# Kernel optimization log

Measured on AMD Instinct MI355X. Metric: run time of the kernel, lower is better.

## Reference

```python
import jax, jax.numpy as jnp
import numpy as np

D_MODEL = 1024
N_HEADS = 16
D_HEAD = D_MODEL // N_HEADS
D_FF = 4096
B, T = 2, 2048


def layer_norm(x, gamma, beta, eps=1e-5):
    mu = jnp.mean(x, axis=-1, keepdims=True)
    var = jnp.var(x, axis=-1, keepdims=True)
    return (x - mu) * jax.lax.rsqrt(var + eps) * gamma + beta


def setup_inputs() -> dict:
    key = jax.random.key(0)
    ks = jax.random.split(key, 8)
    s = D_MODEL ** -0.5
    return {
        "x": jax.random.normal(ks[0], (B, T, D_MODEL), dtype=jnp.float32),
        "w_qkv": jax.random.normal(ks[1], (D_MODEL, 3 * D_MODEL), dtype=jnp.float32) * s,
        "w_out": jax.random.normal(ks[2], (D_MODEL, D_MODEL), dtype=jnp.float32) * s,
        "ln1_g": jnp.ones((D_MODEL,), jnp.float32),
        "ln1_b": jnp.zeros((D_MODEL,), jnp.float32),
        "ln2_g": jnp.ones((D_MODEL,), jnp.float32),
        "ln2_b": jnp.zeros((D_MODEL,), jnp.float32),
        "w1": jax.random.normal(ks[3], (D_MODEL, D_FF), dtype=jnp.float32) * s,
        "b1": jnp.zeros((D_FF,), jnp.float32),
        "w2": jax.random.normal(ks[4], (D_FF, D_MODEL), dtype=jnp.float32) * (D_FF ** -0.5),
        "b2": jnp.zeros((D_MODEL,), jnp.float32),
    }


def reference(x, w_qkv, w_out, ln1_g, ln1_b, ln2_g, ln2_b, w1, b1, w2, b2):
    Bb, Tt, C = x.shape
    h = layer_norm(x, ln1_g, ln1_b)
    qkv = h @ w_qkv  # [B,T,3C]
    q, k, v = jnp.split(qkv, 3, axis=-1)

    def heads(t):  # [B,T,C] -> [B,H,T,Dh]
        return t.reshape(Bb, Tt, N_HEADS, D_HEAD).transpose(0, 2, 1, 3)

    q, k, v = heads(q), heads(k), heads(v)
    scale = D_HEAD ** -0.5
    attn = jnp.einsum("bhqd,bhkd->bhqk", q, k) * scale
    causal = jnp.tril(jnp.ones((Tt, Tt), dtype=bool))
    attn = jnp.where(causal[None, None], attn, -jnp.inf)
    attn = jax.nn.softmax(attn, axis=-1)
    out = jnp.einsum("bhqk,bhkd->bhqd", attn, v)
    out = out.transpose(0, 2, 1, 3).reshape(Bb, Tt, C)
    x = x + out @ w_out
    h2 = layer_norm(x, ln2_g, ln2_b)
    ff = jax.nn.gelu(h2 @ w1 + b1, approximate=False) @ w2 + b2
    return x + ff
```

## Files before the change

kernel.cpp:

```cpp
#include <hip/hip_runtime.h>
#include <hip/hip_bf16.h>
#include <cstdint>

#define DM 1024
#define DFF 4096
#define NB 2
#define TT 2048
#define NH 16
#define DH 64

typedef unsigned short u16;
typedef __bf16 bf16x8 __attribute__((ext_vector_type(8)));
typedef float f32x4 __attribute__((ext_vector_type(4)));

__device__ __forceinline__ u16 f2b(float f) {
    union { float f; unsigned u; } v; v.f = f;
    unsigned u = v.u;
    return (u16)((u + 0x7FFFu + ((u >> 16) & 1u)) >> 16);
}

__device__ __forceinline__ float b2f(u16 u) {
    union { unsigned x; float f; } v;
    v.x = ((unsigned)u) << 16;
    return v.f;
}

__device__ __forceinline__ unsigned cvtpk(float a, float b) {
    unsigned r;
    asm("v_cvt_pk_bf16_f32 %0, %1, %2" : "=v"(r) : "v"(a), "v"(b));
    return r;
}

__device__ __forceinline__ float gelu_fast(float z) {
    const float u = z * z;
    const float w = z * __builtin_fmaf(u, 0.10294324f, 2.3022082f);
    const float e = exp2f(w);
    const float r = __builtin_amdgcn_rcpf(1.0f + e);
    return z - z * r;
}

__device__ __forceinline__ f32x4 mfma_bf16(bf16x8 a, bf16x8 b, f32x4 c) {
    return __builtin_amdgcn_mfma_f32_16x16x32_bf16(a, b, c, 0, 0, 0);
}

__device__ __forceinline__ void gload_lds16(const void* g, void* l) {
    __builtin_amdgcn_global_load_lds((const __attribute__((address_space(1))) unsigned int*)g,
                                     (__attribute__((address_space(3))) unsigned int*)l, 16, 0, 0);
}

__global__ __launch_bounds__(256) void transW(const float* __restrict__ W, u16* __restrict__ Wt,
                                              int K, int N) {
    __shared__ float t[32][33];
    int tx = threadIdx.x & 31, ty = threadIdx.x >> 5;
    int k0 = blockIdx.y * 32, n0 = blockIdx.x * 32;
#pragma unroll
    for (int j = 0; j < 4; ++j)
        t[ty + 8 * j][tx] = W[(size_t)(k0 + ty + 8 * j) * N + n0 + tx];
    __syncthreads();
#pragma unroll
    for (int j = 0; j < 4; ++j)
        Wt[(size_t)(n0 + ty + 8 * j) * K + k0 + tx] = f2b(t[tx][ty + 8 * j]);
}

__global__ __launch_bounds__(256) void ln_kernel(const float* __restrict__ X,
                                                 const float* __restrict__ g,
                                                 const float* __restrict__ bt,
                                                 u16* __restrict__ H) {
    int row = blockIdx.x, tid = threadIdx.x;
    float4 v = ((const float4*)(X + (size_t)row * DM))[tid];
    float s = v.x + v.y + v.z + v.w;
    float ss = v.x * v.x + v.y * v.y + v.z * v.z + v.w * v.w;
#pragma unroll
    for (int off = 32; off >= 1; off >>= 1) {
        s += __shfl_xor(s, off);
        ss += __shfl_xor(ss, off);
    }
    __shared__ float sb[8];
    int w = tid >> 6, lane = tid & 63;
    if (lane == 0) { sb[w] = s; sb[4 + w] = ss; }
    __syncthreads();
    s = sb[0] + sb[1] + sb[2] + sb[3];
    ss = sb[4] + sb[5] + sb[6] + sb[7];
    float mu = s * (1.0f / DM);
    float var = ss * (1.0f / DM) - mu * mu;
    float rstd = rsqrtf(var + 1e-5f);
    float4 gv = ((const float4*)g)[tid];
    float4 bv = ((const float4*)bt)[tid];
    uint2 hv;
    hv.x = cvtpk((v.x - mu) * rstd * gv.x + bv.x, (v.y - mu) * rstd * gv.y + bv.y);
    hv.y = cvtpk((v.z - mu) * rstd * gv.z + bv.z, (v.w - mu) * rstd * gv.w + bv.w);
    ((uint2*)(H + (size_t)row * DM))[tid] = hv;
}

__global__ __launch_bounds__(256) void add3_kernel(float* __restrict__ out,
                                                   const u16* __restrict__ p1,
                                                   const u16* __restrict__ p2,
                                                   const u16* __restrict__ p3, int n4) {
    int idx = blockIdx.x * 256 + threadIdx.x;
    const int stride = gridDim.x * 256;
    for (; idx < n4; idx += stride) {
        float4 a = ((const float4*)out)[idx];
        ushort4 b1 = ((const ushort4*)p1)[idx];
        ushort4 b2 = ((const ushort4*)p2)[idx];
        ushort4 b3 = ((const ushort4*)p3)[idx];
        a.x += b2f(b1.x) + b2f(b2.x) + b2f(b3.x);
        a.y += b2f(b1.y) + b2f(b2.y) + b2f(b3.y);
        a.z += b2f(b1.z) + b2f(b2.z) + b2f(b3.z);
        a.w += b2f(b1.w) + b2f(b2.w) + b2f(b3.w);
        ((float4*)out)[idx] = a;
    }
}

template <int MODE>
__global__ __launch_bounds__(512, 2) void gemm256(
    const u16* __restrict__ A, const u16* __restrict__ Bt, int M, int N, int K,
    u16* __restrict__ oq, u16* __restrict__ ok, u16* __restrict__ vt,
    const float* __restrict__ bias, u16* __restrict__ outbf) {
    __shared__ __align__(16) u16 Alds[2][256][64];
    __shared__ __align__(16) u16 Blds[2][256][64];
    const int tid = threadIdx.x;
    const int lane = tid & 63, w = tid >> 6;
    const int wm = w >> 2, wn = w & 3;
    const int l15 = lane & 15, lg = lane >> 4;
    int bid = blockIdx.x + gridDim.x * blockIdx.y;
    const int nwg = gridDim.x * gridDim.y;
    bid = (bid & 7) * (nwg >> 3) + (bid >> 3);
    const int bm = (bid / gridDim.x) * 256, bn = (bid % gridDim.x) * 256;
    const int srow = tid >> 3, pch = tid & 7;
    const int lc = pch ^ (srow & 7);

    const u16* Ap = A + (size_t)(bm + srow) * K + lc * 8;
    const u16* Bp = Bt + (size_t)(bn + srow) * K + lc * 8;

    f32x4 acc[8][4] = {};
    bf16x8 bf[4][2];
    const int NT = K >> 6;

#define SA256(buf, t)                                                           \
    {                                                                           \
        _Pragma("unroll") for (int j = 0; j < 4; ++j)                           \
            gload_lds16(Ap + (size_t)(64 * j) * K + (t) * 64,                   \
                        &Alds[buf][srow + 64 * j][pch * 8]);                    \
    }
#define SB256(buf, t)                                                           \
    {                                                                           \
        _Pragma("unroll") for (int j = 0; j < 4; ++j)                           \
            gload_lds16(Bp + (size_t)(64 * j) * K + (t) * 64,                   \
                        &Blds[buf][srow + 64 * j][pch * 8]);                    \
    }

#define PHASE(BUF, P, STAGE, WAIT)                                              \
    {                                                                           \
        bf16x8 af[2][2];                                                        \
        _Pragma("unroll") for (int i = 0; i < 2; ++i) {                         \
            const int row = wm * 128 + (2 * (P) + i) * 16 + l15;                \
            _Pragma("unroll") for (int ks = 0; ks < 2; ++ks)                    \
                af[i][ks] =                                                     \
                    *(const bf16x8*)&Alds[BUF][row][((ks * 4 + lg) ^ (row & 7)) * 8]; \
        }                                                                       \
        if constexpr ((P) == 0) {                                               \
            _Pragma("unroll") for (int nf = 0; nf < 4; ++nf) {                  \
                const int row = wn * 64 + nf * 16 + l15;                        \
                _Pragma("unroll") for (int ks = 0; ks < 2; ++ks)                \
                    bf[nf][ks] =                                                \
                        *(const bf16x8*)&Blds[BUF][row][((ks * 4 + lg) ^ (row & 7)) * 8]; \
            }                                                                   \
        }                                                                       \
        STAGE;                                                                  \
        WAIT;                                                                   \
        __builtin_amdgcn_s_barrier();                                           \
        asm volatile("s_waitcnt lgkmcnt(0)" ::: "memory");                      \
        __builtin_amdgcn_sched_barrier(0);                                      \
        __builtin_amdgcn_s_setprio(1);                                          \
        _Pragma("unroll") for (int i = 0; i < 2; ++i)                           \
            _Pragma("unroll") for (int nf = 0; nf < 4; ++nf)                    \
                _Pragma("unroll") for (int ks = 0; ks < 2; ++ks)                \
                    acc[2 * (P) + i][nf] =                                      \
                        mfma_bf16(af[i][ks], bf[nf][ks], acc[2 * (P) + i][nf]); \
        __builtin_amdgcn_s_setprio(0);                                          \
        __builtin_amdgcn_s_barrier();                                           \
    }

    SB256(0, 0);
    SA256(0, 0);
    SB256(1, 1);
    asm volatile("s_waitcnt vmcnt(4)" ::: "memory");
    __builtin_amdgcn_sched_barrier(0);
    __builtin_amdgcn_s_barrier();

    for (int it = 0; it < (NT >> 1); ++it) {
        const int t0 = 2 * it;
        const bool more = (t0 + 2 < NT);
        PHASE(0, 0, { SA256(1, t0 + 1); }, {});
        PHASE(0, 1, { if (more) SB256(0, t0 + 2); }, {});
        PHASE(0, 2, {}, {});
        PHASE(0, 3, {}, {
            if (more) { asm volatile("s_waitcnt vmcnt(4)" ::: "memory"); }
            else { asm volatile("s_waitcnt vmcnt(0)" ::: "memory"); }
            __builtin_amdgcn_sched_barrier(0);
        });
        PHASE(1, 0, { if (more) SA256(0, t0 + 2); }, {});
        PHASE(1, 1, { if (more) SB256(1, t0 + 3); }, {});
        PHASE(1, 2, {}, {});
        PHASE(1, 3, {}, {
            if (more) {
                asm volatile("s_waitcnt vmcnt(4)" ::: "memory");
                __builtin_amdgcn_sched_barrier(0);
            }
        });
    }
#undef PHASE
#undef SA256
#undef SB256

    const int m0 = bm + wm * 128, n0 = bn + wn * 64;
#pragma unroll
    for (int mi = 0; mi < 8; ++mi) {
#pragma unroll
        for (int ni = 0; ni < 4; ++ni) {
            if constexpr (MODE == 0) {
                const int n = n0 + ni * 16 + l15;
                const int which = n >> 10;
                const int hh = (n >> 6) & 15, d = n & 63;
                const int mbase = m0 + mi * 16 + 4 * lg;
                const int bb = mbase >> 11, t = mbase & 2047;
                if (which == 2) {
                    uint2 pv;
                    pv.x = cvtpk(acc[mi][ni][0], acc[mi][ni][1]);
                    pv.y = cvtpk(acc[mi][ni][2], acc[mi][ni][3]);
                    *(uint2*)(vt + (((size_t)(bb * NH + hh)) * DH + d) * TT + t) = pv;
                } else {
                    u16* dst = which == 0 ? oq : ok;
                    const float sc = which == 0 ? 0.18033688f : 1.0f;
                    const unsigned p01 = cvtpk(acc[mi][ni][0] * sc, acc[mi][ni][1] * sc);
                    const unsigned p23 = cvtpk(acc[mi][ni][2] * sc, acc[mi][ni][3] * sc);
                    u16* db = dst + (((size_t)(bb * NH + hh)) * TT + t) * DH + d;
                    db[0] = (u16)p01;
                    db[DH] = (u16)(p01 >> 16);
                    db[2 * DH] = (u16)p23;
                    db[3 * DH] = (u16)(p23 >> 16);
                }
            } else {
                const int n = n0 + ni * 16 + l15;
                const float bn_ = bias[n];
                const float g0 = gelu_fast(acc[mi][ni][0] + bn_);
                const float g1 = gelu_fast(acc[mi][ni][1] + bn_);
                const float g2 = gelu_fast(acc[mi][ni][2] + bn_);
                const float g3 = gelu_fast(acc[mi][ni][3] + bn_);
                const unsigned p01 = cvtpk(g0, g1);
                const unsigned p23 = cvtpk(g2, g3);
                u16* db = outbf + (size_t)(m0 + mi * 16 + 4 * lg) * N + n;
                db[0] = (u16)p01;
                db[N] = (u16)(p01 >> 16);
                db[2 * N] = (u16)p23;
                db[3 * N] = (u16)(p23 >> 16);
            }
        }
    }
}

template <int MODE, int DBUF, int SPLIT>
__global__ __launch_bounds__(256) void gemm_kernel(
    const u16* __restrict__ A, const u16* __restrict__ Bt, int M, int N, int K,
    const float* __restrict__ resid, float* __restrict__ outf,
    const float* __restrict__ bias,
    u16* __restrict__ pb1, u16* __restrict__ pb2, u16* __restrict__ pb3) {
    __shared__ __align__(16) u16 Alds[DBUF + 1][128][64];
    __shared__ __align__(16) u16 Blds[DBUF + 1][128][64];
    const int tid = threadIdx.x;
    const int lane = tid & 63;
    const int w = tid >> 6;
    const int wr = w >> 1, wc = w & 1;
    int bid = blockIdx.x + gridDim.x * blockIdx.y;
    const int nwg = gridDim.x * gridDim.y;
    bid = (bid & 7) * (nwg >> 3) + (bid >> 3);
    int mrow = bid / gridDim.x;
    int ks = 0;
    if constexpr (SPLIT > 1) {
        const int mtiles = (nwg / gridDim.x) / SPLIT;
        ks = mrow / mtiles;
        mrow -= ks * mtiles;
    }
    const int bm = mrow * 128, bn = (bid % gridDim.x) * 128;
    const int kbeg = SPLIT > 1 ? ks * (K / SPLIT) : 0;
    const int kend = kbeg + K / SPLIT;
    const int l15 = lane & 15, lg = lane >> 4;
    const int srow = tid >> 3, pch = tid & 7;
    const int lc = pch ^ (srow & 7);

    f32x4 acc[4][4] = {};
    const u16* Ap = A + (size_t)(bm + srow) * K + lc * 8;
    const u16* Bp = Bt + (size_t)(bn + srow) * K + lc * 8;

#define STAGE(buf, k0)                                                          \
    {                                                                           \
        _Pragma("unroll") for (int i = 0; i < 4; ++i) {                         \
            gload_lds16(Ap + (size_t)(32 * i) * K + (k0), &Alds[buf][srow + 32 * i][pch * 8]); \
            gload_lds16(Bp + (size_t)(32 * i) * K + (k0), &Blds[buf][srow + 32 * i][pch * 8]); \
        }                                                                       \
    }

#define COMPUTE(buf)                                                            \
    {                                                                           \
        _Pragma("unroll") for (int kk = 0; kk < 2; ++kk) {                      \
            bf16x8 af[4], bfr[4];                                               \
            _Pragma("unroll") for (int f = 0; f < 4; ++f) {                     \
                const int ar = wr * 64 + f * 16 + l15;                          \
                const int br = wc * 64 + f * 16 + l15;                          \
                const int kch = kk * 4 + lg;                                    \
                af[f] = *(const bf16x8*)&Alds[buf][ar][(kch ^ (ar & 7)) * 8];   \
                bfr[f] = *(const bf16x8*)&Blds[buf][br][(kch ^ (br & 7)) * 8];  \
            }                                                                   \
            _Pragma("unroll") for (int mi = 0; mi < 4; ++mi)                    \
                _Pragma("unroll") for (int ni = 0; ni < 4; ++ni)                \
                    acc[mi][ni] = mfma_bf16(af[mi], bfr[ni], acc[mi][ni]);      \
        }                                                                       \
    }

    if constexpr (DBUF == 0) {
        for (int k0 = kbeg; k0 < kend; k0 += 64) {
            STAGE(0, k0);
            __syncthreads();
            COMPUTE(0);
            __syncthreads();
        }
    } else {
        STAGE(0, kbeg);
        for (int k0 = kbeg; k0 < kend; k0 += 64) {
            const int cur = ((k0 - kbeg) >> 6) & 1;
            if (k0 + 64 < kend) {
                STAGE(cur ^ 1, k0 + 64);
                asm volatile("s_waitcnt vmcnt(8)" ::: "memory");
            } else {
                asm volatile("s_waitcnt vmcnt(0)" ::: "memory");
            }
            __builtin_amdgcn_sched_barrier(0);
            __builtin_amdgcn_s_barrier();
            __builtin_amdgcn_sched_barrier(0);
            COMPUTE(cur);
            __builtin_amdgcn_s_barrier();
        }
    }
#undef STAGE
#undef COMPUTE

    const int m0 = bm + wr * 64, n0 = bn + wc * 64;
#pragma unroll
    for (int mi = 0; mi < 4; ++mi) {
#pragma unroll
        for (int ni = 0; ni < 4; ++ni) {
            const int n = n0 + ni * 16 + l15;
            if (MODE == 3 && SPLIT > 1 && ks > 0) {
                u16* pb = ks == 1 ? pb1 : (ks == 2 ? pb2 : pb3);
                const unsigned q01 = cvtpk(acc[mi][ni][0], acc[mi][ni][1]);
                const unsigned q23 = cvtpk(acc[mi][ni][2], acc[mi][ni][3]);
                u16* db = pb + (size_t)(m0 + mi * 16 + 4 * lg) * N + n;
                db[0] = (u16)q01;
                db[N] = (u16)(q01 >> 16);
                db[2 * N] = (u16)q23;
                db[3 * N] = (u16)(q23 >> 16);
            } else {
#pragma unroll
                for (int r = 0; r < 4; ++r) {
                    const int m = m0 + mi * 16 + 4 * lg + r;
                    const float v = acc[mi][ni][r];
                    const size_t o = (size_t)m * N + n;
                    if constexpr (MODE == 1) {
                        outf[o] = resid[o] + v;
                    } else {
                        outf[o] = resid[o] + v + bias[n];
                    }
                }
            }
        }
    }
}

__global__ __launch_bounds__(256) void attn_kernel(const u16* __restrict__ Q,
                                                   const u16* __restrict__ Kg,
                                                   const u16* __restrict__ Vtg,
                                                   u16* __restrict__ O) {
    __shared__ __align__(16) u16 Klds[4][64][64];
    __shared__ __align__(16) u16 Vlds[4][64][64];
    const int tid = threadIdx.x, lane = tid & 63, w = tid >> 6;
    const int l15 = lane & 15, lg = lane >> 4;

    int id = blockIdx.x + (blockIdx.y << 4);
    int sw = (id & 7) * 64 + (id >> 3);
    const int p = sw & 15, bh = sw >> 4;
    const size_t base = (size_t)bh * TT * DH;
    const int b = bh >> 4, hh = bh & 15;

    const int srow = tid >> 3, pch = tid & 7;
    const int lc = pch ^ (srow & 7);

    const int src0 = (((2 * lg) & 3) << 4) | l15;
    const int src1 = src0 + 16;
    const bool hi = (lg >> 1) != 0;

#define ASTAGE(buf, kv)                                                                     \
    {                                                                                       \
        gload_lds16(Kg + base + (size_t)((kv) * 64 + srow) * DH + lc * 8,                   \
                    &Klds[buf][srow][pch * 8]);                                             \
        gload_lds16(Kg + base + (size_t)((kv) * 64 + srow + 32) * DH + lc * 8,              \
                    &Klds[buf][srow + 32][pch * 8]);                                        \
        gload_lds16(Vtg + base + (size_t)srow * TT + (kv) * 64 + lc * 8,                    \
                    &Vlds[buf][srow][pch * 8]);                                             \
        gload_lds16(Vtg + base + (size_t)(srow + 32) * TT + (kv) * 64 + lc * 8,             \
                    &Vlds[buf][srow + 32][pch * 8]);                                        \
    }

    for (int half = 0; half < 2; ++half) {
        const int qt = half ? (31 - p) : p;
        const int nkv = qt + 1;
        const int qrow = qt * 64 + w * 16 + l15;
        uint4 qu0 = *(const uint4*)(Q + base + (size_t)qrow * DH + 8 * lg);
        uint4 qu1 = *(const uint4*)(Q + base + (size_t)qrow * DH + 32 + 8 * lg);
        asm volatile("" : "+v"(qu0.x), "+v"(qu0.y), "+v"(qu0.z), "+v"(qu0.w),
                          "+v"(qu1.x), "+v"(qu1.y), "+v"(qu1.z), "+v"(qu1.w));
        const bf16x8 qf0 = *(const bf16x8*)&qu0;
        const bf16x8 qf1 = *(const bf16x8*)&qu1;

        f32x4 o[4] = {};
        float lsum = 0.0f;

        auto compute_tile = [&](int buf, bool masked, int kvi) {
            f32x4 s[4] = {};
            __builtin_amdgcn_s_setprio(1);
#pragma unroll
            for (int nf = 0; nf < 4; ++nf) {
                const int row = nf * 16 + l15;
                bf16x8 kb0 = *(const bf16x8*)&Klds[buf][row][(lg ^ (l15 & 7)) * 8];
                bf16x8 kb1 = *(const bf16x8*)&Klds[buf][row][((4 + lg) ^ (l15 & 7)) * 8];
                s[nf] = mfma_bf16(kb0, qf0, s[nf]);
                s[nf] = mfma_bf16(kb1, qf1, s[nf]);
            }
            __builtin_amdgcn_s_setprio(0);

            if (masked) {
#pragma unroll
                for (int nf = 0; nf < 4; ++nf) {
                    const int tg = kvi * 64 + nf * 16 + 4 * lg;
#pragma unroll
                    for (int r = 0; r < 4; ++r)
                        if (tg + r > qrow) s[nf][r] = -1e30f;
                }
            }

            float ps = 0.0f;
#pragma unroll
            for (int nf = 0; nf < 4; ++nf) {
#pragma unroll
                for (int r = 0; r < 4; ++r) {
                    const float pp = exp2f(s[nf][r]);
                    s[nf][r] = pp;
                    ps += pp;
                }
            }
            lsum += ps;

            unsigned pk[4][2];
#pragma unroll
            for (int nf = 0; nf < 4; ++nf) {
                pk[nf][0] = cvtpk(s[nf][0], s[nf][1]);
                pk[nf][1] = cvtpk(s[nf][2], s[nf][3]);
            }
            bf16x8 pa[2];
#pragma unroll
            for (int kf = 0; kf < 2; ++kf) {
                unsigned a0 = __shfl((int)pk[2 * kf][0], src0);
                unsigned a1 = __shfl((int)pk[2 * kf][1], src0);
                unsigned a2 = __shfl((int)pk[2 * kf][0], src1);
                unsigned a3 = __shfl((int)pk[2 * kf][1], src1);
                unsigned c0 = __shfl((int)pk[2 * kf + 1][0], src0);
                unsigned c1 = __shfl((int)pk[2 * kf + 1][1], src0);
                unsigned c2 = __shfl((int)pk[2 * kf + 1][0], src1);
                unsigned c3 = __shfl((int)pk[2 * kf + 1][1], src1);
                uint4 wv;
                wv.x = hi ? c0 : a0;
                wv.y = hi ? c1 : a1;
                wv.z = hi ? c2 : a2;
                wv.w = hi ? c3 : a3;
                pa[kf] = *(const bf16x8*)&wv;
            }

            __builtin_amdgcn_s_setprio(1);
#pragma unroll
            for (int nf = 0; nf < 4; ++nf) {
                const int row = nf * 16 + l15;
                bf16x8 vb0 = *(const bf16x8*)&Vlds[buf][row][(lg ^ (l15 & 7)) * 8];
                bf16x8 vb1 = *(const bf16x8*)&Vlds[buf][row][((4 + lg) ^ (l15 & 7)) * 8];
                o[nf] = mfma_bf16(vb0, pa[0], o[nf]);
                o[nf] = mfma_bf16(vb1, pa[1], o[nf]);
            }
            __builtin_amdgcn_s_setprio(0);
        };

        ASTAGE(0, 0);
        if (nkv > 1) ASTAGE(1, 1);

        for (int kv = 0; kv < nkv; kv += 2) {
            int nst = 0;
            if (kv + 2 < nkv) { ASTAGE((kv + 2) & 3, kv + 2); nst += 4; }
            if (kv + 3 < nkv) { ASTAGE((kv + 3) & 3, kv + 3); nst += 4; }
            if (nst == 8)
                asm volatile("s_waitcnt vmcnt(8)" ::: "memory");
            else if (nst == 4)
                asm volatile("s_waitcnt vmcnt(4)" ::: "memory");
            else
                asm volatile("s_waitcnt vmcnt(0)" ::: "memory");
            __builtin_amdgcn_sched_barrier(0);
            __builtin_amdgcn_s_barrier();
            __builtin_amdgcn_sched_barrier(0);

            compute_tile(kv & 3, kv == qt, kv);
            if (kv + 1 < nkv) compute_tile((kv + 1) & 3, kv + 1 == qt, kv + 1);

            __builtin_amdgcn_s_barrier();
        }

        lsum += __shfl_xor(lsum, 16);
        lsum += __shfl_xor(lsum, 32);
        const float linv = 1.0f / lsum;
#pragma unroll
        for (int nf = 0; nf < 4; ++nf) {
            uint2 pv;
            pv.x = cvtpk(o[nf][0] * linv, o[nf][1] * linv);
            pv.y = cvtpk(o[nf][2] * linv, o[nf][3] * linv);
            *(uint2*)(O + ((size_t)b * TT + qrow) * DM + hh * DH + nf * 16 + 4 * lg) = pv;
        }
    }
#undef ASTAGE
}

extern "C" void kernel_launch(void* const* d_in, const int* in_sizes, int n_in,
                              void* d_out, int out_size, void* d_ws, size_t ws_size,
                              hipStream_t stream) {
    const float* x = (const float*)d_in[0];
    const float* wqkv = (const float*)d_in[1];
    const float* wout = (const float*)d_in[2];
    const float* ln1g = (const float*)d_in[3];
    const float* ln1b = (const float*)d_in[4];
    const float* ln2g = (const float*)d_in[5];
    const float* ln2b = (const float*)d_in[6];
    const float* w1 = (const float*)d_in[7];
    const float* b1 = (const float*)d_in[8];
    const float* w2 = (const float*)d_in[9];
    const float* b2 = (const float*)d_in[10];
    float* out = (float*)d_out;
    char* ws = (char*)d_ws;

    u16* wqkv_t = (u16*)(ws + 0);
    u16* wout_t = (u16*)(ws + 6291456);
    u16* w1_t   = (u16*)(ws + 8388608);
    u16* w2_t   = (u16*)(ws + 16777216);
    u16* h_bf   = (u16*)(ws + 25165824);
    u16* q_bf   = (u16*)(ws + 33554432);
    u16* k_bf   = (u16*)(ws + 41943040);
    u16* vt_bf  = (u16*)(ws + 50331648);
    u16* at_bf  = (u16*)(ws + 58720256);
    float* x1   = (float*)(ws + 67108864);
    u16* ff1_bf = q_bf;
    u16* pb1 = (u16*)(ws + 0);
    u16* pb2 = (u16*)(ws + 8388608);
    u16* pb3 = (u16*)(ws + 25165824);

    transW<<<dim3(96, 32), 256, 0, stream>>>(wqkv, wqkv_t, 1024, 3072);
    transW<<<dim3(32, 32), 256, 0, stream>>>(wout, wout_t, 1024, 1024);
    transW<<<dim3(128, 32), 256, 0, stream>>>(w1, w1_t, 1024, 4096);
    transW<<<dim3(32, 128), 256, 0, stream>>>(w2, w2_t, 4096, 1024);

    ln_kernel<<<4096, 256, 0, stream>>>(x, ln1g, ln1b, h_bf);

    gemm256<0><<<dim3(12, 16), 512, 0, stream>>>(h_bf, wqkv_t, 4096, 3072, 1024,
                                                 q_bf, k_bf, vt_bf, nullptr, nullptr);

    attn_kernel<<<dim3(16, 32), 256, 0, stream>>>(q_bf, k_bf, vt_bf, at_bf);

    gemm_kernel<1, 1, 1><<<dim3(8, 32), 256, 0, stream>>>(at_bf, wout_t, 4096, 1024, 1024,
                                                          x, x1, nullptr,
                                                          nullptr, nullptr, nullptr);

    ln_kernel<<<4096, 256, 0, stream>>>(x1, ln2g, ln2b, h_bf);

    gemm256<2><<<dim3(16, 16), 512, 0, stream>>>(h_bf, w1_t, 4096, 4096, 1024,
                                                 nullptr, nullptr, nullptr, b1, ff1_bf);

    gemm_kernel<3, 0, 4><<<dim3(8, 128), 256, 0, stream>>>(ff1_bf, w2_t, 4096, 1024, 4096,
                                                           x1, out, b2,
                                                           pb1, pb2, pb3);

    add3_kernel<<<2048, 256, 0, stream>>>(out, pb1, pb2, pb3, 4096 * 1024 / 4);
}
```

Measured before the change: 247.0 us.

## Run FFN down-projection split-K GEMM on the 256x256 tiled gemm256 kernel

Adds split-K support and a residual-plus-bias epilogue to the 256x256 tiled gemm256 kernel. The FFN second GEMM (K=4096) now uses it with 4 K-splits instead of the single-buffered 128x128 gemm_kernel. The goal is more data reuse per tile and a pipelined main loop for the largest-K GEMM. The trade-off is fewer workgroups (256) and larger per-block register and LDS use. gemm_kernel loses its split and DBUF template paths and keeps only the double-buffered path.

```diff
diff --git a/kernel.cpp b/kernel.cpp
--- a/kernel.cpp
+++ b/kernel.cpp
@@ -111,11 +111,13 @@
     }
 }
 
-template <int MODE>
+template <int MODE, int SPLIT>
 __global__ __launch_bounds__(512, 2) void gemm256(
     const u16* __restrict__ A, const u16* __restrict__ Bt, int M, int N, int K,
     u16* __restrict__ oq, u16* __restrict__ ok, u16* __restrict__ vt,
-    const float* __restrict__ bias, u16* __restrict__ outbf) {
+    const float* __restrict__ bias, u16* __restrict__ outbf,
+    const float* __restrict__ resid, float* __restrict__ outf,
+    u16* __restrict__ pb1, u16* __restrict__ pb2, u16* __restrict__ pb3) {
     __shared__ __align__(16) u16 Alds[2][256][64];
     __shared__ __align__(16) u16 Blds[2][256][64];
     const int tid = threadIdx.x;
@@ -125,16 +127,24 @@
     int bid = blockIdx.x + gridDim.x * blockIdx.y;
     const int nwg = gridDim.x * gridDim.y;
     bid = (bid & 7) * (nwg >> 3) + (bid >> 3);
-    const int bm = (bid / gridDim.x) * 256, bn = (bid % gridDim.x) * 256;
+    int mrow = bid / gridDim.x;
+    int ks = 0;
+    if constexpr (SPLIT > 1) {
+        const int mtiles = (nwg / gridDim.x) / SPLIT;
+        ks = mrow / mtiles;
+        mrow -= ks * mtiles;
+    }
+    const int bm = mrow * 256, bn = (bid % gridDim.x) * 256;
+    const int kbeg = SPLIT > 1 ? ks * (K / SPLIT) : 0;
     const int srow = tid >> 3, pch = tid & 7;
     const int lc = pch ^ (srow & 7);
 
-    const u16* Ap = A + (size_t)(bm + srow) * K + lc * 8;
-    const u16* Bp = Bt + (size_t)(bn + srow) * K + lc * 8;
+    const u16* Ap = A + (size_t)(bm + srow) * K + kbeg + lc * 8;
+    const u16* Bp = Bt + (size_t)(bn + srow) * K + kbeg + lc * 8;
 
     f32x4 acc[8][4] = {};
     bf16x8 bf[4][2];
-    const int NT = K >> 6;
+    const int NT = (K / SPLIT) >> 6;
 
 #define SA256(buf, t)                                                           \
     {                                                                           \
@@ -154,16 +164,16 @@
         bf16x8 af[2][2];                                                        \
         _Pragma("unroll") for (int i = 0; i < 2; ++i) {                         \
             const int row = wm * 128 + (2 * (P) + i) * 16 + l15;                \
-            _Pragma("unroll") for (int ks = 0; ks < 2; ++ks)                    \
-                af[i][ks] =                                                     \
-                    *(const bf16x8*)&Alds[BUF][row][((ks * 4 + lg) ^ (row & 7)) * 8]; \
+            _Pragma("unroll") for (int ks_ = 0; ks_ < 2; ++ks_)                 \
+                af[i][ks_] =                                                    \
+                    *(const bf16x8*)&Alds[BUF][row][((ks_ * 4 + lg) ^ (row & 7)) * 8]; \
         }                                                                       \
         if constexpr ((P) == 0) {                                               \
             _Pragma("unroll") for (int nf = 0; nf < 4; ++nf) {                  \
                 const int row = wn * 64 + nf * 16 + l15;                        \
-                _Pragma("unroll") for (int ks = 0; ks < 2; ++ks)                \
-                    bf[nf][ks] =                                                \
-                        *(const bf16x8*)&Blds[BUF][row][((ks * 4 + lg) ^ (row & 7)) * 8]; \
+                _Pragma("unroll") for (int ks_ = 0; ks_ < 2; ++ks_)             \
+                    bf[nf][ks_] =                                               \
+                        *(const bf16x8*)&Blds[BUF][row][((ks_ * 4 + lg) ^ (row & 7)) * 8]; \
             }                                                                   \
         }                                                                       \
         STAGE;                                                                  \
@@ -174,9 +184,9 @@
         __builtin_amdgcn_s_setprio(1);                                          \
         _Pragma("unroll") for (int i = 0; i < 2; ++i)                           \
             _Pragma("unroll") for (int nf = 0; nf < 4; ++nf)                    \
-                _Pragma("unroll") for (int ks = 0; ks < 2; ++ks)                \
+                _Pragma("unroll") for (int ks_ = 0; ks_ < 2; ++ks_)             \
                     acc[2 * (P) + i][nf] =                                      \
-                        mfma_bf16(af[i][ks], bf[nf][ks], acc[2 * (P) + i][nf]); \
+                        mfma_bf16(af[i][ks_], bf[nf][ks_], acc[2 * (P) + i][nf]); \
         __builtin_amdgcn_s_setprio(0);                                          \
         __builtin_amdgcn_s_barrier();                                           \
     }
@@ -240,7 +250,7 @@
                     db[2 * DH] = (u16)p23;
                     db[3 * DH] = (u16)(p23 >> 16);
                 }
-            } else {
+            } else if constexpr (MODE == 2) {
                 const int n = n0 + ni * 16 + l15;
                 const float bn_ = bias[n];
                 const float g0 = gelu_fast(acc[mi][ni][0] + bn_);
@@ -254,19 +264,38 @@
                 db[N] = (u16)(p01 >> 16);
                 db[2 * N] = (u16)p23;
                 db[3 * N] = (u16)(p23 >> 16);
+            } else {
+                const int n = n0 + ni * 16 + l15;
+                if (SPLIT > 1 && ks > 0) {
+                    u16* pb = ks == 1 ? pb1 : (ks == 2 ? pb2 : pb3);
+                    const unsigned q01 = cvtpk(acc[mi][ni][0], acc[mi][ni][1]);
+                    const unsigned q23 = cvtpk(acc[mi][ni][2], acc[mi][ni][3]);
+                    u16* db = pb + (size_t)(m0 + mi * 16 + 4 * lg) * N + n;
+                    db[0] = (u16)q01;
+                    db[N] = (u16)(q01 >> 16);
+                    db[2 * N] = (u16)q23;
+                    db[3 * N] = (u16)(q23 >> 16);
+                } else {
+                    const float bn_ = bias[n];
+#pragma unroll
+                    for (int r = 0; r < 4; ++r) {
+                        const int m = m0 + mi * 16 + 4 * lg + r;
+                        const size_t o = (size_t)m * N + n;
+                        outf[o] = resid[o] + acc[mi][ni][r] + bn_;
+                    }
+                }
             }
         }
     }
 }
 
-template <int MODE, int DBUF, int SPLIT>
+template <int MODE>
 __global__ __launch_bounds__(256) void gemm_kernel(
     const u16* __restrict__ A, const u16* __restrict__ Bt, int M, int N, int K,
     const float* __restrict__ resid, float* __restrict__ outf,
-    const float* __restrict__ bias,
-    u16* __restrict__ pb1, u16* __restrict__ pb2, u16* __restrict__ pb3) {
-    __shared__ __align__(16) u16 Alds[DBUF + 1][128][64];
-    __shared__ __align__(16) u16 Blds[DBUF + 1][128][64];
+    const float* __restrict__ bias) {
+    __shared__ __align__(16) u16 Alds[2][128][64];
+    __shared__ __align__(16) u16 Blds[2][128][64];
     const int tid = threadIdx.x;
     const int lane = tid & 63;
     const int w = tid >> 6;
@@ -274,16 +303,7 @@
     int bid = blockIdx.x + gridDim.x * blockIdx.y;
     const int nwg = gridDim.x * gridDim.y;
     bid = (bid & 7) * (nwg >> 3) + (bid >> 3);
-    int mrow = bid / gridDim.x;
-    int ks = 0;
-    if constexpr (SPLIT > 1) {
-        const int mtiles = (nwg / gridDim.x) / SPLIT;
-        ks = mrow / mtiles;
-        mrow -= ks * mtiles;
-    }
-    const int bm = mrow * 128, bn = (bid % gridDim.x) * 128;
-    const int kbeg = SPLIT > 1 ? ks * (K / SPLIT) : 0;
-    const int kend = kbeg + K / SPLIT;
+    const int bm = (bid / gridDim.x) * 128, bn = (bid % gridDim.x) * 128;
     const int l15 = lane & 15, lg = lane >> 4;
     const int srow = tid >> 3, pch = tid & 7;
     const int lc = pch ^ (srow & 7);
@@ -317,29 +337,20 @@
         }                                                                       \
     }
 
-    if constexpr (DBUF == 0) {
-        for (int k0 = kbeg; k0 < kend; k0 += 64) {
-            STAGE(0, k0);
-            __syncthreads();
-            COMPUTE(0);
-            __syncthreads();
+    STAGE(0, 0);
+    for (int k0 = 0; k0 < K; k0 += 64) {
+        const int cur = (k0 >> 6) & 1;
+        if (k0 + 64 < K) {
+            STAGE(cur ^ 1, k0 + 64);
+            asm volatile("s_waitcnt vmcnt(8)" ::: "memory");
+        } else {
+            asm volatile("s_waitcnt vmcnt(0)" ::: "memory");
         }
-    } else {
-        STAGE(0, kbeg);
-        for (int k0 = kbeg; k0 < kend; k0 += 64) {
-            const int cur = ((k0 - kbeg) >> 6) & 1;
-            if (k0 + 64 < kend) {
-                STAGE(cur ^ 1, k0 + 64);
-                asm volatile("s_waitcnt vmcnt(8)" ::: "memory");
-            } else {
-                asm volatile("s_waitcnt vmcnt(0)" ::: "memory");
-            }
-            __builtin_amdgcn_sched_barrier(0);
-            __builtin_amdgcn_s_barrier();
-            __builtin_amdgcn_sched_barrier(0);
-            COMPUTE(cur);
-            __builtin_amdgcn_s_barrier();
-        }
+        __builtin_amdgcn_sched_barrier(0);
+        __builtin_amdgcn_s_barrier();
+        __builtin_amdgcn_sched_barrier(0);
+        COMPUTE(cur);
+        __builtin_amdgcn_s_barrier();
     }
 #undef STAGE
 #undef COMPUTE
@@ -350,26 +361,15 @@
 #pragma unroll
         for (int ni = 0; ni < 4; ++ni) {
             const int n = n0 + ni * 16 + l15;
-            if (MODE == 3 && SPLIT > 1 && ks > 0) {
-                u16* pb = ks == 1 ? pb1 : (ks == 2 ? pb2 : pb3);
-                const unsigned q01 = cvtpk(acc[mi][ni][0], acc[mi][ni][1]);
-                const unsigned q23 = cvtpk(acc[mi][ni][2], acc[mi][ni][3]);
-                u16* db = pb + (size_t)(m0 + mi * 16 + 4 * lg) * N + n;
-                db[0] = (u16)q01;
-                db[N] = (u16)(q01 >> 16);
-                db[2 * N] = (u16)q23;
-                db[3 * N] = (u16)(q23 >> 16);
-            } else {
-#pragma unroll
-                for (int r = 0; r < 4; ++r) {
-                    const int m = m0 + mi * 16 + 4 * lg + r;
-                    const float v = acc[mi][ni][r];
-                    const size_t o = (size_t)m * N + n;
-                    if constexpr (MODE == 1) {
-                        outf[o] = resid[o] + v;
-                    } else {
-                        outf[o] = resid[o] + v + bias[n];
-                    }
+#pragma unroll
+            for (int r = 0; r < 4; ++r) {
+                const int m = m0 + mi * 16 + 4 * lg + r;
+                const float v = acc[mi][ni][r];
+                const size_t o = (size_t)m * N + n;
+                if constexpr (MODE == 1) {
+                    outf[o] = resid[o] + v;
+                } else {
+                    outf[o] = resid[o] + v + bias[n];
                 }
             }
         }
@@ -572,23 +572,27 @@
 
     ln_kernel<<<4096, 256, 0, stream>>>(x, ln1g, ln1b, h_bf);
 
-    gemm256<0><<<dim3(12, 16), 512, 0, stream>>>(h_bf, wqkv_t, 4096, 3072, 1024,
-                                                 q_bf, k_bf, vt_bf, nullptr, nullptr);
+    gemm256<0, 1><<<dim3(12, 16), 512, 0, stream>>>(h_bf, wqkv_t, 4096, 3072, 1024,
+                                                    q_bf, k_bf, vt_bf, nullptr, nullptr,
+                                                    nullptr, nullptr,
+                                                    nullptr, nullptr, nullptr);
 
     attn_kernel<<<dim3(16, 32), 256, 0, stream>>>(q_bf, k_bf, vt_bf, at_bf);
 
-    gemm_kernel<1, 1, 1><<<dim3(8, 32), 256, 0, stream>>>(at_bf, wout_t, 4096, 1024, 1024,
-                                                          x, x1, nullptr,
-                                                          nullptr, nullptr, nullptr);
+    gemm_kernel<1><<<dim3(8, 32), 256, 0, stream>>>(at_bf, wout_t, 4096, 1024, 1024,
+                                                    x, x1, nullptr);
 
     ln_kernel<<<4096, 256, 0, stream>>>(x1, ln2g, ln2b, h_bf);
 
-    gemm256<2><<<dim3(16, 16), 512, 0, stream>>>(h_bf, w1_t, 4096, 4096, 1024,
-                                                 nullptr, nullptr, nullptr, b1, ff1_bf);
-
-    gemm_kernel<3, 0, 4><<<dim3(8, 128), 256, 0, stream>>>(ff1_bf, w2_t, 4096, 1024, 4096,
-                                                           x1, out, b2,
-                                                           pb1, pb2, pb3);
+    gemm256<2, 1><<<dim3(16, 16), 512, 0, stream>>>(h_bf, w1_t, 4096, 4096, 1024,
+                                                    nullptr, nullptr, nullptr, b1, ff1_bf,
+                                                    nullptr, nullptr,
+                                                    nullptr, nullptr, nullptr);
+
+    gemm256<3, 4><<<dim3(4, 64), 512, 0, stream>>>(ff1_bf, w2_t, 4096, 1024, 4096,
+                                                   nullptr, nullptr, nullptr, b2, nullptr,
+                                                   x1, out,
+                                                   pb1, pb2, pb3);
 
     add3_kernel<<<2048, 256, 0, stream>>>(out, pb1, pb2, pb3, 4096 * 1024 / 4);
 }
```

New measurement: 239.9 us. 2.9% less time.
